# Kernel tuning notes

Hardware: AMD Instinct MI355X
Metric: run time of the kernel (lower is better)

## Reference

```python
import jax, jax.numpy as jnp
import numpy as np

B, S, H, NH = 2, 2048, 2048, 32
HD = H // NH  # 64

def _causal_mask(b, s, dtype=jnp.float32):
    neg = jnp.finfo(dtype).min
    m = jnp.where(jnp.tril(jnp.ones((s, s), dtype=bool)), 0.0, neg).astype(dtype)
    return jnp.broadcast_to(m[None, None], (b, 1, s, s))

def setup_inputs() -> dict:
    key = jax.random.key(0)
    k1, k2, k3, k4, k5 = jax.random.split(key, 5)
    scale = 1.0 / np.sqrt(H)
    return {
        "hidden_states": jax.random.normal(k1, (B, S, H), jnp.float32),
        "attention_mask": _causal_mask(B, S),
        "Wq": jax.random.normal(k2, (H, H), jnp.float32) * scale,
        "Wk": jax.random.normal(k3, (H, H), jnp.float32) * scale,
        "Wv": jax.random.normal(k4, (H, H), jnp.float32) * scale,
        "Wo": jax.random.normal(k5, (H, H), jnp.float32) * scale,
    }

def reference(hidden_states, attention_mask, Wq, Wk, Wv, Wo):
    b, s, _ = hidden_states.shape
    dt = hidden_states.dtype
    def proj(W):  # torch Linear: x @ W.T -> [b, nh, s, hd]
        return (hidden_states @ W.T).reshape(b, s, NH, HD).transpose(0, 2, 1, 3)
    q, k, v = proj(Wq), proj(Wk), proj(Wv)
    attn = jnp.einsum('bhqd,bhkd->bhqk', q, k) / np.sqrt(HD)
    attn = attn + attention_mask
    attn = jnp.maximum(attn, jnp.finfo(attn.dtype).min)
    attn = jax.nn.softmax(attn.astype(jnp.float32), axis=-1).astype(dt)
    out = jnp.einsum('bhqk,bhkd->bhqd', attn, v)
    out = out.transpose(0, 2, 1, 3).reshape(b, s, H)
    return out @ Wo.T
```

## Files before the change

kernel.cpp:

```cpp
#include <hip/hip_runtime.h>
#include <hip/hip_bf16.h>
#include <stdint.h>

#define S_LEN 2048
#define NHEAD 32
#define HDIM  64

using bf16x8 = __attribute__((ext_vector_type(8))) short;
using f32x4  = __attribute__((ext_vector_type(4))) float;
using f32x16 = __attribute__((ext_vector_type(16))) float;

__device__ __forceinline__ uint16_t f2bf(float f) {
  union { float f; uint32_t u; } c; c.f = f;
  uint32_t u = c.u;
  return (uint16_t)((u + 0x7FFFu + ((u >> 16) & 1u)) >> 16);
}

__device__ __forceinline__ void load_lds16(const void* g, void* l) {
  __builtin_amdgcn_global_load_lds(
      (const __attribute__((address_space(1))) void*)g,
      (__attribute__((address_space(3))) void*)l, 16, 0, 0);
}

__device__ __forceinline__ f32x16 mfma32(bf16x8 a, bf16x8 b, f32x16 c) {
  return __builtin_amdgcn_mfma_f32_32x32x16_bf16(a, b, c, 0, 0, 0);
}

__device__ __forceinline__ uint32_t cvtpk(float lo, float hi_) {
  uint32_t d;
  asm("v_cvt_pk_bf16_f32 %0, %1, %2" : "=v"(d) : "v"(lo), "v"(hi_));
  return d;
}
__device__ __forceinline__ void plswap(uint32_t& a, uint32_t& b) {
  asm volatile("v_permlane32_swap_b32 %0, %1" : "+v"(a), "+v"(b));
}

__global__ __launch_bounds__(256) void conv_batch(
    const float* __restrict__ X, const float* __restrict__ Wq,
    const float* __restrict__ Wk, const float* __restrict__ Wv,
    uint16_t* __restrict__ Xbf, uint16_t* __restrict__ Wqk,
    uint16_t* __restrict__ Wvb) {
  int i = blockIdx.x * 256 + threadIdx.x;
  const float* src; uint16_t* dst; int o;
  if (i < 2097152)      { src = X;  dst = Xbf;           o = i; }
  else if (i < 3145728) { src = Wq; dst = Wqk;           o = i - 2097152; }
  else if (i < 4194304) { src = Wk; dst = Wqk + 4194304; o = i - 3145728; }
  else                  { src = Wv; dst = Wvb;           o = i - 4194304; }
  float4 v = ((const float4*)src)[o];
  uint64_t packed = (uint64_t)f2bf(v.x) | ((uint64_t)f2bf(v.y) << 16) |
                    ((uint64_t)f2bf(v.z) << 32) | ((uint64_t)f2bf(v.w) << 48);
  ((uint64_t*)dst)[o] = packed;
}

__global__ __launch_bounds__(256) void conv_f32_bf16(
    const float* __restrict__ in, uint16_t* __restrict__ out, int n4) {
  int i = blockIdx.x * 256 + threadIdx.x;
  if (i < n4) {
    float4 v = ((const float4*)in)[i];
    uint64_t packed = (uint64_t)f2bf(v.x) | ((uint64_t)f2bf(v.y) << 16) |
                      ((uint64_t)f2bf(v.z) << 32) | ((uint64_t)f2bf(v.w) << 48);
    ((uint64_t*)out)[i] = packed;
  }
}

__global__ __launch_bounds__(512, 2) void gemm_qk(
    const uint16_t* __restrict__ A, const uint16_t* __restrict__ Bw,
    uint16_t* __restrict__ Qo, uint16_t* __restrict__ Ko, float qscale) {
  extern __shared__ char smem[];
  const int t = threadIdx.x;
  const int lane = t & 63, w = t >> 6;
  const int lrow = lane & 15, lgrp = lane >> 4;
  const int wr = w >> 2, wc = w & 3;
  const int id = blockIdx.x;
  const int swz = (id & 7) * 32 + (id >> 3);
  const int bm = (swz & 15) * 256, bn = (swz >> 4) * 256;
  constexpr int NT = 2048 / 32;

  const f32x4 zero4 = {0.f, 0.f, 0.f, 0.f};
  f32x4 acc[8][4];
#pragma unroll
  for (int mi = 0; mi < 8; ++mi)
#pragma unroll
    for (int ni = 0; ni < 4; ++ni) acc[mi][ni] = zero4;

  auto stage_mat = [&](const uint16_t* __restrict__ G, int grow0,
                       char* ldsbase, int kt) {
#pragma unroll
    for (int j = 0; j < 2; ++j) {
      const int s = t + j * 512;
      const int row = s >> 2;
      const int sc = (s & 3) ^ ((row >> 1) & 3);
      load_lds16(G + (size_t)(grow0 + row) * 2048 + kt + sc * 8,
                 ldsbase + j * 8192 + w * 1024);
    }
  };
  auto lda = [&](const char* Ab, int mi) -> bf16x8 {
    const int row = wr * 128 + mi * 16 + lrow;
    return *(const bf16x8*)(Ab + row * 64 + ((lgrp ^ ((row >> 1) & 3)) << 4));
  };
  auto ldb = [&](const char* Bb, int ni) -> bf16x8 {
    const int row = wc * 64 + ni * 16 + lrow;
    return *(const bf16x8*)(Bb + row * 64 + ((lgrp ^ ((row >> 1) & 3)) << 4));
  };

  stage_mat(A, bm, smem, 0);
  stage_mat(Bw, bn, smem + 16384, 0);
  stage_mat(A, bm, smem + 32768, 32);
  stage_mat(Bw, bn, smem + 32768 + 16384, 32);

  for (int kt = 0; kt < NT; ++kt) {
    char* cur = smem + (kt % 3) * 32768;
    char* nx2 = smem + ((kt + 2) % 3) * 32768;
    if (kt < NT - 1) asm volatile("s_waitcnt vmcnt(4)" ::: "memory");
    else             asm volatile("s_waitcnt vmcnt(0)" ::: "memory");
    __builtin_amdgcn_s_barrier();

    bf16x8 aF[4], bF[4];
#pragma unroll
    for (int mi = 0; mi < 4; ++mi) aF[mi] = lda(cur, mi);
#pragma unroll
    for (int ni = 0; ni < 4; ++ni) bF[ni] = ldb(cur + 16384, ni);
    if (kt + 2 < NT) stage_mat(A, bm, nx2, (kt + 2) * 32);
    __builtin_amdgcn_s_barrier();
    asm volatile("s_waitcnt lgkmcnt(0)" ::: "memory");
    __builtin_amdgcn_sched_barrier(0);
    __builtin_amdgcn_s_setprio(1);
#pragma unroll
    for (int mi = 0; mi < 4; ++mi)
#pragma unroll
      for (int ni = 0; ni < 4; ++ni)
        acc[mi][ni] = __builtin_amdgcn_mfma_f32_16x16x32_bf16(
            aF[mi], bF[ni], acc[mi][ni], 0, 0, 0);
    __builtin_amdgcn_s_setprio(0);
    __builtin_amdgcn_s_barrier();

    bf16x8 aG[4];
#pragma unroll
    for (int mi = 0; mi < 4; ++mi) aG[mi] = lda(cur, 4 + mi);
    if (kt + 2 < NT) stage_mat(Bw, bn, nx2 + 16384, (kt + 2) * 32);
    __builtin_amdgcn_s_barrier();
    asm volatile("s_waitcnt lgkmcnt(0)" ::: "memory");
    __builtin_amdgcn_sched_barrier(0);
    __builtin_amdgcn_s_setprio(1);
#pragma unroll
    for (int mi = 0; mi < 4; ++mi)
#pragma unroll
      for (int ni = 0; ni < 4; ++ni)
        acc[4 + mi][ni] = __builtin_amdgcn_mfma_f32_16x16x32_bf16(
            aG[mi], bF[ni], acc[4 + mi][ni], 0, 0, 0);
    __builtin_amdgcn_s_setprio(0);
  }

  const bool isQ = (bn < 2048);
#pragma unroll
  for (int mi = 0; mi < 8; ++mi) {
#pragma unroll
    for (int ni = 0; ni < 4; ++ni) {
      const int n = bn + wc * 64 + ni * 16 + lrow;
      const int n2 = isQ ? n : (n - 2048);
      const int h = n2 >> 6, d = n2 & 63;
#pragma unroll
      for (int r = 0; r < 4; ++r) {
        const int m = bm + wr * 128 + mi * 16 + lgrp * 4 + r;
        const int b = m >> 11, s = m & 2047;
        const size_t off = (((size_t)(b * NHEAD + h) * S_LEN + s) * HDIM) + d;
        if (isQ) Qo[off] = f2bf(acc[mi][ni][r] * qscale);
        else     Ko[off] = f2bf(acc[mi][ni][r]);
      }
    }
  }
}

template<int MODE>
__global__ __launch_bounds__(256, 3) void gemm_nt(
    const uint16_t* __restrict__ A, const uint16_t* __restrict__ B,
    void* __restrict__ C, int M, int N, int K, float scale) {
  __shared__ __align__(16) char smem[3][16384];

  const int t = threadIdx.x;
  const int lane = t & 63, w = t >> 6;
  const int lrow = lane & 15, lgrp = lane >> 4;
  const int bm = blockIdx.y * 128, bn = blockIdx.x * 128;
  const int wm = (w >> 1) * 64, wn = (w & 1) * 64;
  const int NT = K / 32;

  const f32x4 zero4 = {0.f, 0.f, 0.f, 0.f};
  f32x4 acc[4][4];
#pragma unroll
  for (int mi = 0; mi < 4; ++mi)
#pragma unroll
    for (int ni = 0; ni < 4; ++ni) acc[mi][ni] = zero4;

  auto stage_mat = [&](const uint16_t* __restrict__ G, int grow0,
                       char* ldsbase, int kt) {
#pragma unroll
    for (int j = 0; j < 2; ++j) {
      const int s = t + j * 256;
      const int row = s >> 2;
      const int sc = (s & 3) ^ ((row >> 1) & 3);
      load_lds16(G + (size_t)(grow0 + row) * K + kt + sc * 8,
                 ldsbase + j * 4096 + w * 1024);
    }
  };
  auto ldf = [&](const char* Mb, int base, int i) -> bf16x8 {
    const int row = base + i * 16 + lrow;
    return *(const bf16x8*)(Mb + row * 64 + ((lgrp ^ ((row >> 1) & 3)) << 4));
  };

  stage_mat(A, bm, smem[0], 0);
  stage_mat(B, bn, smem[0] + 8192, 0);
  stage_mat(A, bm, smem[1], 32);
  stage_mat(B, bn, smem[1] + 8192, 32);

  for (int kt = 0; kt < NT; ++kt) {
    char* cur = smem[kt % 3];
    if (kt < NT - 1) asm volatile("s_waitcnt vmcnt(4)" ::: "memory");
    else             asm volatile("s_waitcnt vmcnt(0)" ::: "memory");
    __builtin_amdgcn_s_barrier();

    if (kt + 2 < NT) {
      char* nx2 = smem[(kt + 2) % 3];
      stage_mat(A, bm, nx2, (kt + 2) * 32);
      stage_mat(B, bn, nx2 + 8192, (kt + 2) * 32);
    }

    bf16x8 aF[4], bF[4];
#pragma unroll
    for (int mi = 0; mi < 4; ++mi) aF[mi] = ldf(cur, wm, mi);
#pragma unroll
    for (int ni = 0; ni < 4; ++ni) bF[ni] = ldf(cur + 8192, wn, ni);
#pragma unroll
    for (int mi = 0; mi < 4; ++mi)
#pragma unroll
      for (int ni = 0; ni < 4; ++ni)
        acc[mi][ni] = __builtin_amdgcn_mfma_f32_16x16x32_bf16(
            aF[mi], bF[ni], acc[mi][ni], 0, 0, 0);
  }

#pragma unroll
  for (int mi = 0; mi < 4; ++mi) {
#pragma unroll
    for (int ni = 0; ni < 4; ++ni) {
      const int n = bn + wn + ni * 16 + lrow;
#pragma unroll
      for (int r = 0; r < 4; ++r) {
        const int m = bm + wm + mi * 16 + lgrp * 4 + r;
        const float v = acc[mi][ni][r] * scale;
        if (MODE == 2) {
          ((float*)C)[(size_t)m * N + n] = v;
        } else {
          const int h = m >> 6, d = m & 63;
          const int b = n >> 11, s = n & 2047;
          ((uint16_t*)C)[(((size_t)(b * NHEAD + h) * HDIM + d) * S_LEN) + s] =
              f2bf(v);
        }
      }
    }
  }
}

__global__ __launch_bounds__(256, 3) void attn_kernel(
    const uint16_t* __restrict__ Q, const uint16_t* __restrict__ K,
    const uint16_t* __restrict__ Vt, uint16_t* __restrict__ O) {
  __shared__ __align__(16) uint16_t Ks[2][64 * 64];
  __shared__ __align__(16) uint16_t Vs[2][64 * 64];
  __shared__ float Ls[4][32];

  const int t = threadIdx.x, lane = t & 63, w = t >> 6;
  const int qcol = lane & 31, hi = lane >> 5;
  const int id = blockIdx.x;
  const int bh = (id & 7) * 8 + ((id >> 3) & 7);
  const int p = id >> 6;
  const int b = bh >> 5, h = bh & 31;

  const uint16_t* Qbh = Q + (size_t)bh * S_LEN * HDIM;
  const uint16_t* Kbh = K + (size_t)bh * S_LEN * HDIM;
  const uint16_t* Vbh = Vt + (size_t)bh * HDIM * S_LEN;

  const int srow = lane >> 3;
  const int schunk = (lane & 7) ^ srow;

  auto stage = [&](int k0, int bi) {
#pragma unroll
    for (int j = 0; j < 2; ++j) {
      const int r = j * 32 + w * 8 + srow;
      load_lds16(Kbh + (size_t)(k0 + r) * HDIM + schunk * 8,
                 (char*)&Ks[bi][0] + j * 4096 + w * 1024);
      load_lds16(Vbh + (size_t)r * S_LEN + k0 + schunk * 8,
                 (char*)&Vs[bi][0] + j * 4096 + w * 1024);
    }
  };

  for (int pass = 0; pass < 2; ++pass) {
    const int jq = pass ? (15 - p) : p;
    const int qw = jq * 128 + w * 32;
    const int qg = qw + qcol;

    bf16x8 qB[4];
    {
      const uint16_t* qp = Qbh + (size_t)(qw + qcol) * HDIM + hi * 8;
#pragma unroll
      for (int j = 0; j < 4; ++j) qB[j] = *(const bf16x8*)(qp + 16 * j);
    }

    f32x16 oacc0, oacc1;
#pragma unroll
    for (int r = 0; r < 16; ++r) { oacc0[r] = 0.f; oacc1[r] = 0.f; }
    float lsum = 0.f;

    const int nt = 2 * jq + 2;
    for (int kt = 0; kt < nt; ++kt) {
      const int cur = kt & 1;
      const int k0 = kt * 64;
      if (kt == 0) { __syncthreads(); stage(0, 0); }
      __syncthreads();
      if (kt + 1 < nt) stage((kt + 1) * 64, cur ^ 1);

      if (k0 <= qw + 31) {
        const char* Kc = (const char*)&Ks[cur][0];
        const char* Vc = (const char*)&Vs[cur][0];

        f32x16 s0, s1;
#pragma unroll
        for (int r = 0; r < 16; ++r) { s0[r] = 0.f; s1[r] = 0.f; }
        const int rk0 = qcol, rk1 = 32 + qcol;
        const int x0 = rk0 & 7;
        __builtin_amdgcn_s_setprio(1);
#pragma unroll
        for (int j = 0; j < 4; ++j) {
          bf16x8 kf0 = *(const bf16x8*)(Kc + rk0 * 128 + (((2*j+hi) ^ x0) << 4));
          bf16x8 kf1 = *(const bf16x8*)(Kc + rk1 * 128 + (((2*j+hi) ^ x0) << 4));
          s0 = mfma32(kf0, qB[j], s0);
          s1 = mfma32(kf1, qB[j], s1);
        }
        __builtin_amdgcn_s_setprio(0);

        if (k0 + 63 > qw) {
#pragma unroll
          for (int r = 0; r < 16; ++r) {
            const int krow = (r & 3) + 8 * (r >> 2) + 4 * hi;
            s0[r] = (k0 + krow <= qg) ? __expf(s0[r]) : 0.f;
            s1[r] = (k0 + 32 + krow <= qg) ? __expf(s1[r]) : 0.f;
            lsum += s0[r] + s1[r];
          }
        } else {
#pragma unroll
          for (int r = 0; r < 16; ++r) {
            s0[r] = __expf(s0[r]);
            s1[r] = __expf(s1[r]);
            lsum += s0[r] + s1[r];
          }
        }

        bf16x8 paf[4];
#pragma unroll
        for (int tt = 0; tt < 4; ++tt) {
          const int o = 8 * (tt & 1);
          uint32_t a0, a1, a2, a3;
          if (tt < 2) {
            a0 = cvtpk(s0[o + 0], s0[o + 1]);
            a1 = cvtpk(s0[o + 2], s0[o + 3]);
            a2 = cvtpk(s0[o + 4], s0[o + 5]);
            a3 = cvtpk(s0[o + 6], s0[o + 7]);
          } else {
            a0 = cvtpk(s1[o + 0], s1[o + 1]);
            a1 = cvtpk(s1[o + 2], s1[o + 3]);
            a2 = cvtpk(s1[o + 4], s1[o + 5]);
            a3 = cvtpk(s1[o + 6], s1[o + 7]);
          }
          plswap(a0, a2);
          plswap(a1, a3);
          union { uint32_t u[4]; bf16x8 v; } pk;
          pk.u[0] = a0; pk.u[1] = a1; pk.u[2] = a2; pk.u[3] = a3;
          paf[tt] = pk.v;
        }

        __builtin_amdgcn_s_setprio(1);
#pragma unroll
        for (int tt = 0; tt < 4; ++tt) {
          const int c = 2 * tt + hi;
          bf16x8 v0f = *(const bf16x8*)(Vc + rk0 * 128 + ((c ^ x0) << 4));
          bf16x8 v1f = *(const bf16x8*)(Vc + rk1 * 128 + ((c ^ x0) << 4));
          oacc0 = mfma32(paf[tt], v0f, oacc0);
          oacc1 = mfma32(paf[tt], v1f, oacc1);
        }
        __builtin_amdgcn_s_setprio(0);
      }
    }

    lsum += __shfl_xor(lsum, 32, 64);
    if (hi == 0) Ls[w][qcol] = 1.0f / lsum;

#pragma unroll
    for (int r = 0; r < 16; ++r) {
      const int qrow = (r & 3) + 8 * (r >> 2) + 4 * hi;
      const float inv = Ls[w][qrow];
      const size_t base = ((size_t)b * S_LEN + qw + qrow) * 2048 + h * 64;
      O[base + qcol] = f2bf(oacc0[r] * inv);
      O[base + 32 + qcol] = f2bf(oacc1[r] * inv);
    }
  }
}

extern "C" void kernel_launch(void* const* d_in, const int* in_sizes, int n_in,
                              void* d_out, int out_size, void* d_ws,
                              size_t ws_size, hipStream_t stream) {
  const float* X  = (const float*)d_in[0];
  const float* Wq = (const float*)d_in[2];
  const float* Wk = (const float*)d_in[3];
  const float* Wv = (const float*)d_in[4];
  const float* Wo = (const float*)d_in[5];
  float* out = (float*)d_out;

  char* ws = (char*)d_ws;
  uint16_t* Xbf = (uint16_t*)ws;
  uint16_t* Wqk = (uint16_t*)(ws + 16777216);
  uint16_t* Qb  = (uint16_t*)(ws + 33554432);
  uint16_t* Kb  = (uint16_t*)(ws + 50331648);
  uint16_t* Wsm = (uint16_t*)(ws + 67108864);
  uint16_t* Vtb = Wqk;
  uint16_t* Ob  = Xbf;

  const float qscale = 0.125f;

  hipFuncSetAttribute((const void*)gemm_qk,
                      hipFuncAttributeMaxDynamicSharedMemorySize, 98304);

  conv_batch<<<20480, 256, 0, stream>>>(X, Wq, Wk, Wv, Xbf, Wqk, Wsm);
  gemm_qk<<<256, 512, 98304, stream>>>(Xbf, Wqk, Qb, Kb, qscale);
  gemm_nt<1><<<dim3(32, 16), 256, 0, stream>>>(Wsm, Xbf, Vtb, 2048, 4096, 2048, 1.0f);
  attn_kernel<<<dim3(512), 256, 0, stream>>>(Qb, Kb, Vtb, Ob);
  conv_f32_bf16<<<4096, 256, 0, stream>>>(Wo, Wsm, 1048576);
  gemm_nt<2><<<dim3(16, 32), 256, 0, stream>>>(Ob, Wsm, out, 4096, 2048, 2048, 1.0f);
}
```

Measured before the change: 230.4 us.

## Share K/V tiles between paired query blocks in attention and fuse Wo conversion

The attention kernel now processes its two query tiles (p and 15-p) together. Each staged K/V tile is loaded once and used by both, instead of running two separate passes that re-stage the shared prefix. The Wo fp32-to-bf16 conversion is folded into the initial batched conversion kernel, which removes one launch. Holding two sets of accumulators raises register pressure, so the occupancy hint in launch_bounds is dropped and occupancy may fall.

```diff
diff --git a/kernel.cpp b/kernel.cpp
--- a/kernel.cpp
+++ b/kernel.cpp
@@ -38,29 +38,20 @@
 __global__ __launch_bounds__(256) void conv_batch(
     const float* __restrict__ X, const float* __restrict__ Wq,
     const float* __restrict__ Wk, const float* __restrict__ Wv,
-    uint16_t* __restrict__ Xbf, uint16_t* __restrict__ Wqk,
-    uint16_t* __restrict__ Wvb) {
+    const float* __restrict__ Wo, uint16_t* __restrict__ Xbf,
+    uint16_t* __restrict__ Wqk, uint16_t* __restrict__ Wvb,
+    uint16_t* __restrict__ Wob) {
   int i = blockIdx.x * 256 + threadIdx.x;
   const float* src; uint16_t* dst; int o;
   if (i < 2097152)      { src = X;  dst = Xbf;           o = i; }
   else if (i < 3145728) { src = Wq; dst = Wqk;           o = i - 2097152; }
   else if (i < 4194304) { src = Wk; dst = Wqk + 4194304; o = i - 3145728; }
-  else                  { src = Wv; dst = Wvb;           o = i - 4194304; }
+  else if (i < 5242880) { src = Wv; dst = Wvb;           o = i - 4194304; }
+  else                  { src = Wo; dst = Wob;           o = i - 5242880; }
   float4 v = ((const float4*)src)[o];
   uint64_t packed = (uint64_t)f2bf(v.x) | ((uint64_t)f2bf(v.y) << 16) |
                     ((uint64_t)f2bf(v.z) << 32) | ((uint64_t)f2bf(v.w) << 48);
   ((uint64_t*)dst)[o] = packed;
-}
-
-__global__ __launch_bounds__(256) void conv_f32_bf16(
-    const float* __restrict__ in, uint16_t* __restrict__ out, int n4) {
-  int i = blockIdx.x * 256 + threadIdx.x;
-  if (i < n4) {
-    float4 v = ((const float4*)in)[i];
-    uint64_t packed = (uint64_t)f2bf(v.x) | ((uint64_t)f2bf(v.y) << 16) |
-                      ((uint64_t)f2bf(v.z) << 32) | ((uint64_t)f2bf(v.w) << 48);
-    ((uint64_t*)out)[i] = packed;
-  }
 }
 
 __global__ __launch_bounds__(512, 2) void gemm_qk(
@@ -259,7 +250,7 @@
   }
 }
 
-__global__ __launch_bounds__(256, 3) void attn_kernel(
+__global__ __launch_bounds__(256) void attn_kernel(
     const uint16_t* __restrict__ Q, const uint16_t* __restrict__ K,
     const uint16_t* __restrict__ Vt, uint16_t* __restrict__ O) {
   __shared__ __align__(16) uint16_t Ks[2][64 * 64];
@@ -291,115 +282,157 @@
     }
   };
 
-  for (int pass = 0; pass < 2; ++pass) {
-    const int jq = pass ? (15 - p) : p;
-    const int qw = jq * 128 + w * 32;
-    const int qg = qw + qcol;
-
-    bf16x8 qB[4];
-    {
-      const uint16_t* qp = Qbh + (size_t)(qw + qcol) * HDIM + hi * 8;
-#pragma unroll
-      for (int j = 0; j < 4; ++j) qB[j] = *(const bf16x8*)(qp + 16 * j);
-    }
-
-    f32x16 oacc0, oacc1;
-#pragma unroll
-    for (int r = 0; r < 16; ++r) { oacc0[r] = 0.f; oacc1[r] = 0.f; }
-    float lsum = 0.f;
-
-    const int nt = 2 * jq + 2;
-    for (int kt = 0; kt < nt; ++kt) {
-      const int cur = kt & 1;
-      const int k0 = kt * 64;
-      if (kt == 0) { __syncthreads(); stage(0, 0); }
-      __syncthreads();
-      if (kt + 1 < nt) stage((kt + 1) * 64, cur ^ 1);
-
-      if (k0 <= qw + 31) {
-        const char* Kc = (const char*)&Ks[cur][0];
-        const char* Vc = (const char*)&Vs[cur][0];
-
-        f32x16 s0, s1;
-#pragma unroll
-        for (int r = 0; r < 16; ++r) { s0[r] = 0.f; s1[r] = 0.f; }
-        const int rk0 = qcol, rk1 = 32 + qcol;
-        const int x0 = rk0 & 7;
-        __builtin_amdgcn_s_setprio(1);
-#pragma unroll
-        for (int j = 0; j < 4; ++j) {
-          bf16x8 kf0 = *(const bf16x8*)(Kc + rk0 * 128 + (((2*j+hi) ^ x0) << 4));
-          bf16x8 kf1 = *(const bf16x8*)(Kc + rk1 * 128 + (((2*j+hi) ^ x0) << 4));
-          s0 = mfma32(kf0, qB[j], s0);
-          s1 = mfma32(kf1, qB[j], s1);
-        }
-        __builtin_amdgcn_s_setprio(0);
-
-        if (k0 + 63 > qw) {
-#pragma unroll
-          for (int r = 0; r < 16; ++r) {
-            const int krow = (r & 3) + 8 * (r >> 2) + 4 * hi;
-            s0[r] = (k0 + krow <= qg) ? __expf(s0[r]) : 0.f;
-            s1[r] = (k0 + 32 + krow <= qg) ? __expf(s1[r]) : 0.f;
-            lsum += s0[r] + s1[r];
-          }
-        } else {
-#pragma unroll
-          for (int r = 0; r < 16; ++r) {
-            s0[r] = __expf(s0[r]);
-            s1[r] = __expf(s1[r]);
-            lsum += s0[r] + s1[r];
-          }
-        }
-
-        bf16x8 paf[4];
-#pragma unroll
-        for (int tt = 0; tt < 4; ++tt) {
-          const int o = 8 * (tt & 1);
-          uint32_t a0, a1, a2, a3;
-          if (tt < 2) {
-            a0 = cvtpk(s0[o + 0], s0[o + 1]);
-            a1 = cvtpk(s0[o + 2], s0[o + 3]);
-            a2 = cvtpk(s0[o + 4], s0[o + 5]);
-            a3 = cvtpk(s0[o + 6], s0[o + 7]);
-          } else {
-            a0 = cvtpk(s1[o + 0], s1[o + 1]);
-            a1 = cvtpk(s1[o + 2], s1[o + 3]);
-            a2 = cvtpk(s1[o + 4], s1[o + 5]);
-            a3 = cvtpk(s1[o + 6], s1[o + 7]);
-          }
-          plswap(a0, a2);
-          plswap(a1, a3);
-          union { uint32_t u[4]; bf16x8 v; } pk;
-          pk.u[0] = a0; pk.u[1] = a1; pk.u[2] = a2; pk.u[3] = a3;
-          paf[tt] = pk.v;
-        }
-
-        __builtin_amdgcn_s_setprio(1);
-#pragma unroll
-        for (int tt = 0; tt < 4; ++tt) {
-          const int c = 2 * tt + hi;
-          bf16x8 v0f = *(const bf16x8*)(Vc + rk0 * 128 + ((c ^ x0) << 4));
-          bf16x8 v1f = *(const bf16x8*)(Vc + rk1 * 128 + ((c ^ x0) << 4));
-          oacc0 = mfma32(paf[tt], v0f, oacc0);
-          oacc1 = mfma32(paf[tt], v1f, oacc1);
-        }
-        __builtin_amdgcn_s_setprio(0);
-      }
-    }
-
+  const int qtA = p, qtB = 15 - p;
+  const int qwA = qtA * 128 + w * 32, qwB = qtB * 128 + w * 32;
+  const int qgA = qwA + qcol, qgB = qwB + qcol;
+  const int ntA = 2 * qtA + 2, ntB = 2 * qtB + 2;
+
+  bf16x8 qA[4], qB[4];
+  {
+    const uint16_t* qp = Qbh + (size_t)qgA * HDIM + hi * 8;
+#pragma unroll
+    for (int j = 0; j < 4; ++j) qA[j] = *(const bf16x8*)(qp + 16 * j);
+    const uint16_t* qp2 = Qbh + (size_t)qgB * HDIM + hi * 8;
+#pragma unroll
+    for (int j = 0; j < 4; ++j) qB[j] = *(const bf16x8*)(qp2 + 16 * j);
+  }
+
+  f32x16 oA0, oA1, oB0, oB1;
+#pragma unroll
+  for (int r = 0; r < 16; ++r) { oA0[r] = 0.f; oA1[r] = 0.f;
+                                 oB0[r] = 0.f; oB1[r] = 0.f; }
+  float lsA = 0.f, lsB = 0.f;
+
+  const int rk0 = qcol, rk1 = 32 + qcol;
+  const int x0 = qcol & 7;
+
+  auto qk_paf = [&](const bf16x8 (&qf)[4], int qwl, int qgl, int k0,
+                    const char* Kc, bf16x8 (&paf)[4], float& lsum) {
+    f32x16 s0, s1;
+#pragma unroll
+    for (int r = 0; r < 16; ++r) { s0[r] = 0.f; s1[r] = 0.f; }
+    __builtin_amdgcn_s_setprio(1);
+#pragma unroll
+    for (int j = 0; j < 4; ++j) {
+      bf16x8 kf0 = *(const bf16x8*)(Kc + rk0 * 128 + (((2*j+hi) ^ x0) << 4));
+      bf16x8 kf1 = *(const bf16x8*)(Kc + rk1 * 128 + (((2*j+hi) ^ x0) << 4));
+      s0 = mfma32(kf0, qf[j], s0);
+      s1 = mfma32(kf1, qf[j], s1);
+    }
+    __builtin_amdgcn_s_setprio(0);
+    if (k0 + 63 > qwl) {
+#pragma unroll
+      for (int r = 0; r < 16; ++r) {
+        const int krow = (r & 3) + 8 * (r >> 2) + 4 * hi;
+        s0[r] = (k0 + krow <= qgl) ? __expf(s0[r]) : 0.f;
+        s1[r] = (k0 + 32 + krow <= qgl) ? __expf(s1[r]) : 0.f;
+        lsum += s0[r] + s1[r];
+      }
+    } else {
+#pragma unroll
+      for (int r = 0; r < 16; ++r) {
+        s0[r] = __expf(s0[r]);
+        s1[r] = __expf(s1[r]);
+        lsum += s0[r] + s1[r];
+      }
+    }
+#pragma unroll
+    for (int tt = 0; tt < 4; ++tt) {
+      const int o = 8 * (tt & 1);
+      uint32_t a0, a1, a2, a3;
+      if (tt < 2) {
+        a0 = cvtpk(s0[o + 0], s0[o + 1]);
+        a1 = cvtpk(s0[o + 2], s0[o + 3]);
+        a2 = cvtpk(s0[o + 4], s0[o + 5]);
+        a3 = cvtpk(s0[o + 6], s0[o + 7]);
+      } else {
+        a0 = cvtpk(s1[o + 0], s1[o + 1]);
+        a1 = cvtpk(s1[o + 2], s1[o + 3]);
+        a2 = cvtpk(s1[o + 4], s1[o + 5]);
+        a3 = cvtpk(s1[o + 6], s1[o + 7]);
+      }
+      plswap(a0, a2);
+      plswap(a1, a3);
+      union { uint32_t u[4]; bf16x8 v; } pk;
+      pk.u[0] = a0; pk.u[1] = a1; pk.u[2] = a2; pk.u[3] = a3;
+      paf[tt] = pk.v;
+    }
+  };
+
+  auto write_out = [&](const f32x16& o0, const f32x16& o1, int qwl,
+                       float lsum) {
     lsum += __shfl_xor(lsum, 32, 64);
     if (hi == 0) Ls[w][qcol] = 1.0f / lsum;
-
 #pragma unroll
     for (int r = 0; r < 16; ++r) {
       const int qrow = (r & 3) + 8 * (r >> 2) + 4 * hi;
       const float inv = Ls[w][qrow];
-      const size_t base = ((size_t)b * S_LEN + qw + qrow) * 2048 + h * 64;
-      O[base + qcol] = f2bf(oacc0[r] * inv);
-      O[base + 32 + qcol] = f2bf(oacc1[r] * inv);
-    }
-  }
+      const size_t base = ((size_t)b * S_LEN + qwl + qrow) * 2048 + h * 64;
+      O[base + qcol] = f2bf(o0[r] * inv);
+      O[base + 32 + qcol] = f2bf(o1[r] * inv);
+    }
+  };
+
+  stage(0, 0);
+
+  for (int kt = 0; kt < ntA; ++kt) {
+    const int cur = kt & 1;
+    const int k0 = kt * 64;
+    __syncthreads();
+    if (kt + 1 < ntB) stage((kt + 1) * 64, cur ^ 1);
+
+    const char* Kc = (const char*)&Ks[cur][0];
+    const char* Vc = (const char*)&Vs[cur][0];
+    const bool actA = (k0 <= qwA + 31);
+
+    bf16x8 pafA[4], pafB[4];
+    if (actA) qk_paf(qA, qwA, qgA, k0, Kc, pafA, lsA);
+    qk_paf(qB, qwB, qgB, k0, Kc, pafB, lsB);
+
+    __builtin_amdgcn_s_setprio(1);
+#pragma unroll
+    for (int tt = 0; tt < 4; ++tt) {
+      const int c = 2 * tt + hi;
+      bf16x8 v0f = *(const bf16x8*)(Vc + rk0 * 128 + ((c ^ x0) << 4));
+      bf16x8 v1f = *(const bf16x8*)(Vc + rk1 * 128 + ((c ^ x0) << 4));
+      if (actA) {
+        oA0 = mfma32(pafA[tt], v0f, oA0);
+        oA1 = mfma32(pafA[tt], v1f, oA1);
+      }
+      oB0 = mfma32(pafB[tt], v0f, oB0);
+      oB1 = mfma32(pafB[tt], v1f, oB1);
+    }
+    __builtin_amdgcn_s_setprio(0);
+  }
+
+  write_out(oA0, oA1, qwA, lsA);
+
+  for (int kt = ntA; kt < ntB; ++kt) {
+    const int cur = kt & 1;
+    const int k0 = kt * 64;
+    __syncthreads();
+    if (kt + 1 < ntB) stage((kt + 1) * 64, cur ^ 1);
+
+    const char* Kc = (const char*)&Ks[cur][0];
+    const char* Vc = (const char*)&Vs[cur][0];
+    if (k0 > qwB + 31) continue;
+
+    bf16x8 pafB[4];
+    qk_paf(qB, qwB, qgB, k0, Kc, pafB, lsB);
+
+    __builtin_amdgcn_s_setprio(1);
+#pragma unroll
+    for (int tt = 0; tt < 4; ++tt) {
+      const int c = 2 * tt + hi;
+      bf16x8 v0f = *(const bf16x8*)(Vc + rk0 * 128 + ((c ^ x0) << 4));
+      bf16x8 v1f = *(const bf16x8*)(Vc + rk1 * 128 + ((c ^ x0) << 4));
+      oB0 = mfma32(pafB[tt], v0f, oB0);
+      oB1 = mfma32(pafB[tt], v1f, oB1);
+    }
+    __builtin_amdgcn_s_setprio(0);
+  }
+
+  write_out(oB0, oB1, qwB, lsB);
 }
 
 extern "C" void kernel_launch(void* const* d_in, const int* in_sizes, int n_in,
@@ -418,6 +451,7 @@
   uint16_t* Qb  = (uint16_t*)(ws + 33554432);
   uint16_t* Kb  = (uint16_t*)(ws + 50331648);
   uint16_t* Wsm = (uint16_t*)(ws + 67108864);
+  uint16_t* Wob = (uint16_t*)(ws + 75497472);
   uint16_t* Vtb = Wqk;
   uint16_t* Ob  = Xbf;
 
@@ -426,10 +460,9 @@
   hipFuncSetAttribute((const void*)gemm_qk,
                       hipFuncAttributeMaxDynamicSharedMemorySize, 98304);
 
-  conv_batch<<<20480, 256, 0, stream>>>(X, Wq, Wk, Wv, Xbf, Wqk, Wsm);
+  conv_batch<<<24576, 256, 0, stream>>>(X, Wq, Wk, Wv, Wo, Xbf, Wqk, Wsm, Wob);
   gemm_qk<<<256, 512, 98304, stream>>>(Xbf, Wqk, Qb, Kb, qscale);
   gemm_nt<1><<<dim3(32, 16), 256, 0, stream>>>(Wsm, Xbf, Vtb, 2048, 4096, 2048, 1.0f);
   attn_kernel<<<dim3(512), 256, 0, stream>>>(Qb, Kb, Vtb, Ob);
-  conv_f32_bf16<<<4096, 256, 0, stream>>>(Wo, Wsm, 1048576);
-  gemm_nt<2><<<dim3(16, 32), 256, 0, stream>>>(Ob, Wsm, out, 4096, 2048, 2048, 1.0f);
-}
+  gemm_nt<2><<<dim3(16, 32), 256, 0, stream>>>(Ob, Wob, out, 4096, 2048, 2048, 1.0f);
+}
```

After: 251.1 us. 1.09x slower.
